# Performance work log

Hardware: AMD Instinct MI355X
Metric: run time of the kernel (lower is better)

Reference implementation:

```python
import jax, jax.numpy as jnp
import numpy as np

B, C, H, W = 8, 512, 32, 32
NH = 8
DH = C // NH
HW = H * W
LN_EPS = 1e-5
NORM_EPS = 1e-12  # torch F.normalize eps


def setup_inputs() -> dict:
    key = jax.random.key(0)
    ks = jax.random.split(key, 8)
    s = 0.02
    return {
        "x": jax.random.normal(ks[0], (B, C, H, W), dtype=jnp.float32),
        "qkv_w": jax.random.normal(ks[1], (3 * C, C), dtype=jnp.float32) * s,
        "proj_w": jax.random.normal(ks[2], (C, C), dtype=jnp.float32) * s,
        "proj_b": jnp.zeros((C,), dtype=jnp.float32),
        "temperature": jnp.ones((NH, 1, 1), dtype=jnp.float32),
        "ln_g": jnp.ones((C,), dtype=jnp.float32),
        "ln_b": jnp.zeros((C,), dtype=jnp.float32),
        "pos_embed": jax.random.normal(ks[3], (1, HW, C), dtype=jnp.float32) * s,
        "dw_w": jax.random.normal(ks[4], (C, 1, 3, 3), dtype=jnp.float32) * s,
        "dw_b": jnp.zeros((C,), dtype=jnp.float32),
        "pw_w": jax.random.normal(ks[5], (C, C, 1, 1), dtype=jnp.float32) * s,
        "pw_b": jnp.zeros((C,), dtype=jnp.float32),
    }


def _l2norm_tokens(t):
    # normalize along token axis (dim=-2), like F.normalize(t, dim=-2)
    n = jnp.sqrt(jnp.sum(t * t, axis=-2, keepdims=True))
    return t / jnp.maximum(n, NORM_EPS)


def _layernorm(t, g, b):
    mu = jnp.mean(t, axis=-1, keepdims=True)
    var = jnp.mean((t - mu) ** 2, axis=-1, keepdims=True)
    return (t - mu) * jax.lax.rsqrt(var + LN_EPS) * g + b


def _dsconv(t, dw_w, dw_b, pw_w, pw_b):
    # depthwise 3x3 SAME + pointwise 1x1, NCHW / OIHW
    y = jax.lax.conv_general_dilated(
        t, dw_w, window_strides=(1, 1), padding="SAME",
        dimension_numbers=("NCHW", "OIHW", "NCHW"), feature_group_count=C)
    y = y + dw_b[None, :, None, None]
    y = jax.lax.conv_general_dilated(
        y, pw_w, window_strides=(1, 1), padding="SAME",
        dimension_numbers=("NCHW", "OIHW", "NCHW"))
    return y + pw_b[None, :, None, None]


def reference(x, qkv_w, proj_w, proj_b, temperature, ln_g, ln_b, pos_embed, dw_w, dw_b, pw_w, pw_b):
    save = x
    t = jnp.transpose(x.reshape(B, C, HW), (0, 2, 1))  # [B, HW, C]
    t = t + pos_embed
    # qkv projection (no bias)
    qkv = t @ qkv_w.T  # [B, HW, 3C]
    qkv = qkv.reshape(B, HW, 3, NH, DH).transpose(2, 0, 3, 1, 4)  # [3,B,NH,HW,DH]
    q, k, v = qkv[0], qkv[1], qkv[2]
    q = _l2norm_tokens(q)
    k = _l2norm_tokens(k)
    attn = jnp.einsum("bhnd,bhmd->bhnm", q, k) * temperature[None]  # [B,NH,HW,HW]
    attn = jax.nn.softmax(attn, axis=-1)
    o = jnp.einsum("bhnm,bhmd->bhnd", attn, v)  # [B,NH,HW,DH]
    o = o.transpose(0, 2, 1, 3).reshape(B, HW, C)
    o = o @ proj_w.T + proj_b
    o = _layernorm(o, ln_g, ln_b)
    o = jnp.transpose(o, (0, 2, 1)).reshape(B, C, H, W)
    o = o + save
    return o + _dsconv(o, dw_w, dw_b, pw_w, pw_b)
```

## Files before the change

kernel.cpp:

```cpp
#include <hip/hip_runtime.h>
#include <math.h>

#define BB_ 8
#define C_ 512
#define C3_ 1536
#define HW_ 1024
#define NH_ 8
#define DH_ 64
#define HH_ 32
#define WW_ 32

typedef __attribute__((ext_vector_type(8))) short short8;
typedef __attribute__((ext_vector_type(4))) short short4v;
typedef __attribute__((ext_vector_type(8))) unsigned short ushort8;
typedef __attribute__((ext_vector_type(4))) unsigned short ushort4_t;
typedef __attribute__((ext_vector_type(4))) float f32x4;
typedef unsigned short ushort;

__device__ inline ushort f2bf(float f) {
  union { float f; unsigned u; } v;
  v.f = f;
  unsigned r = v.u + 0x7fffu + ((v.u >> 16) & 1u);
  return (ushort)(r >> 16);
}
__device__ inline float bf2f(ushort u) {
  union { unsigned u; float f; } v;
  v.u = ((unsigned)u) << 16;
  return v.f;
}

#define GLD16(gptr, lptr)                                                     \
  __builtin_amdgcn_global_load_lds(                                           \
      (const __attribute__((address_space(1))) unsigned int*)(gptr),          \
      (__attribute__((address_space(3))) unsigned int*)(lptr), 16, 0, 0)

__device__ inline f32x4 pv_mfma(const ushort* vp, short4v pf, f32x4 acc) {
#if __has_builtin(__builtin_amdgcn_mfma_f32_16x16x16_bf16)
  short4v vf = *(const short4v*)vp;
  return __builtin_amdgcn_mfma_f32_16x16x16_bf16(vf, pf, acc, 0, 0, 0);
#elif __has_builtin(__builtin_amdgcn_mfma_f32_16x16x16bf16_1k)
  short4v vf = *(const short4v*)vp;
  return __builtin_amdgcn_mfma_f32_16x16x16bf16_1k(vf, pf, acc, 0, 0, 0);
#else
  short4v v4 = *(const short4v*)vp;
  short8 vf = {v4[0], v4[1], v4[2], v4[3], 0, 0, 0, 0};
  short8 pf8 = {pf[0], pf[1], pf[2], pf[3], 0, 0, 0, 0};
  return __builtin_amdgcn_mfma_f32_16x16x32_bf16(vf, pf8, acc, 0, 0, 0);
#endif
}

__global__ __launch_bounds__(256) void prep_kernel(
    const float* __restrict__ x, const float* __restrict__ pos,
    const float* __restrict__ qkv_w, const float* __restrict__ proj_w,
    const float* __restrict__ pw_w, ushort* __restrict__ t,
    ushort* __restrict__ xT, ushort* __restrict__ wts,
    float* __restrict__ sums) {
  const int bid = blockIdx.x;
  const int tid = threadIdx.x;
  if (bid >= 6144) {
    sums[(bid - 6144) * 256 + tid] = 0.f;
    return;
  }
  if (bid >= 1024) {
    int i = (bid - 1024) * 256 + tid;
    if (i < 786432) wts[i] = f2bf(qkv_w[i]);
    else if (i < 1048576) wts[i] = f2bf(proj_w[i - 786432]);
    else wts[i] = f2bf(pw_w[i - 1048576]);
    return;
  }
  __shared__ float tile[64][65];
  const int n0 = (bid & 15) * 64, c0 = ((bid >> 4) & 7) * 64, b = bid >> 7;
#pragma unroll
  for (int it = 0; it < 4; it++) {
    int c_l = (tid >> 4) + it * 16;
    int n_l4 = (tid & 15) * 4;
    float4 v = *(const float4*)&x[((size_t)(b * C_ + c0 + c_l)) * HW_ + n0 + n_l4];
    tile[c_l][n_l4 + 0] = v.x;
    tile[c_l][n_l4 + 1] = v.y;
    tile[c_l][n_l4 + 2] = v.z;
    tile[c_l][n_l4 + 3] = v.w;
  }
  __syncthreads();
#pragma unroll
  for (int it = 0; it < 4; it++) {
    int n_l = (tid >> 4) + it * 16;
    int c_l4 = (tid & 15) * 4;
    size_t token = (size_t)(b * HW_ + n0 + n_l);
    float4 pv = *(const float4*)&pos[(n0 + n_l) * C_ + c0 + c_l4];
    float xv0 = tile[c_l4 + 0][n_l], xv1 = tile[c_l4 + 1][n_l];
    float xv2 = tile[c_l4 + 2][n_l], xv3 = tile[c_l4 + 3][n_l];
    ushort4_t tb = {f2bf(xv0 + pv.x), f2bf(xv1 + pv.y), f2bf(xv2 + pv.z),
                    f2bf(xv3 + pv.w)};
    ushort4_t xb = {f2bf(xv0), f2bf(xv1), f2bf(xv2), f2bf(xv3)};
    *(ushort4_t*)&t[token * C_ + c0 + c_l4] = tb;
    *(ushort4_t*)&xT[token * C_ + c0 + c_l4] = xb;
  }
}

__global__ __launch_bounds__(256) void gemm_qkv(
    const ushort* __restrict__ A, const ushort* __restrict__ Wm,
    ushort* __restrict__ out, ushort* __restrict__ vt,
    float* __restrict__ qsum, float* __restrict__ ksum) {
  const int N = C3_, K = C_;
  __shared__ alignas(16) ushort As[128 * 32];
  __shared__ alignas(16) ushort Bs[128 * 32];
  const int bn = blockIdx.x * 128, bm = blockIdx.y * 128;
  const int tid = threadIdx.x;
  const int w = tid >> 6, lane = tid & 63;
  const int wm = 64 * (w & 1), wn = 64 * (w >> 1);
  const int l15 = lane & 15, lq = lane >> 4;

  f32x4 acc[4][4];
#pragma unroll
  for (int i = 0; i < 4; i++)
#pragma unroll
    for (int j = 0; j < 4; j++) acc[i][j] = (f32x4){0.f, 0.f, 0.f, 0.f};

  const int srr = lane >> 2, sq1 = lane & 3;

  for (int k0 = 0; k0 < K; k0 += 32) {
    __syncthreads();
#pragma unroll
    for (int j = 0; j < 2; j++) {
      int r = 32 * w + 16 * j + srr;
      int q = (sq1 - (r >> 1)) & 3;
      GLD16(A + (size_t)(bm + r) * K + k0 + q * 8, &As[(32 * w + 16 * j) * 32]);
      GLD16(Wm + (size_t)(bn + r) * K + k0 + q * 8, &Bs[(32 * w + 16 * j) * 32]);
    }
    __syncthreads();
    short8 af[4], bf[4];
#pragma unroll
    for (int nt = 0; nt < 4; nt++) {
      int r = wm + nt * 16 + l15;
      af[nt] = *(const short8*)&As[r * 32 + (((lq + (r >> 1)) & 3) * 8)];
      int c = wn + nt * 16 + l15;
      bf[nt] = *(const short8*)&Bs[c * 32 + (((lq + (c >> 1)) & 3) * 8)];
    }
#pragma unroll
    for (int i = 0; i < 4; i++)
#pragma unroll
      for (int j = 0; j < 4; j++)
        acc[i][j] = __builtin_amdgcn_mfma_f32_16x16x32_bf16(af[i], bf[j],
                                                            acc[i][j], 0, 0, 0);
  }

  const int b = bm >> 10;
  if (bn < 1024) {
#pragma unroll
    for (int j = 0; j < 4; j++) {
      int c = bn + wn + j * 16 + l15;
      float ss = 0.f;
#pragma unroll
      for (int i = 0; i < 4; i++) {
#pragma unroll
        for (int r = 0; r < 4; r++) {
          int m = bm + wm + i * 16 + lq * 4 + r;
          float v = acc[i][j][r];
          ss += v * v;
          out[(size_t)m * N + c] = f2bf(v);
        }
      }
      ss += __shfl_xor(ss, 16);
      ss += __shfl_xor(ss, 32);
      if (lq == 0) {
        if (c < 512) atomicAdd(&qsum[b * 512 + c], ss);
        else atomicAdd(&ksum[b * 512 + c - 512], ss);
      }
    }
  } else {
#pragma unroll
    for (int j = 0; j < 4; j++) {
      int c = bn + wn + j * 16 + l15;
      int hd = c - 1024;
      ushort* vrow = vt + ((size_t)(b * 512 + hd)) * HW_;
#pragma unroll
      for (int i = 0; i < 4; i++) {
        int n0 = (bm & 1023) + wm + i * 16 + lq * 4;
        ushort4_t pv = {f2bf(acc[i][j][0]), f2bf(acc[i][j][1]),
                        f2bf(acc[i][j][2]), f2bf(acc[i][j][3])};
        *(ushort4_t*)&vrow[n0] = pv;
      }
    }
  }
}

template <int EPI>
__global__ __launch_bounds__(256) void gemm_n64(
    const ushort* __restrict__ A, const ushort* __restrict__ Wm,
    const float* __restrict__ bias, void* __restrict__ outv,
    const ushort* __restrict__ resid, int N, int K) {
  __shared__ alignas(16) ushort As[128 * 32];
  __shared__ alignas(16) ushort Bs[64 * 32];
  const int bn = blockIdx.x * 64, bm = blockIdx.y * 128;
  const int tid = threadIdx.x;
  const int w = tid >> 6, lane = tid & 63;
  const int wm = 64 * (w & 1), wn = 32 * (w >> 1);
  const int l15 = lane & 15, lq = lane >> 4;

  f32x4 acc[4][2];
#pragma unroll
  for (int i = 0; i < 4; i++)
#pragma unroll
    for (int j = 0; j < 2; j++) acc[i][j] = (f32x4){0.f, 0.f, 0.f, 0.f};

  const int srr = lane >> 2, sq1 = lane & 3;

  for (int k0 = 0; k0 < K; k0 += 32) {
    __syncthreads();
#pragma unroll
    for (int j = 0; j < 2; j++) {
      int r = 32 * w + 16 * j + srr;
      int q = (sq1 - (r >> 1)) & 3;
      GLD16(A + (size_t)(bm + r) * K + k0 + q * 8, &As[(32 * w + 16 * j) * 32]);
    }
    {
      int r = 16 * w + srr;
      int q = (sq1 - (r >> 1)) & 3;
      GLD16(Wm + (size_t)(bn + r) * K + k0 + q * 8, &Bs[(16 * w) * 32]);
    }
    __syncthreads();
    short8 af[4], bf[2];
#pragma unroll
    for (int nt = 0; nt < 4; nt++) {
      int r = wm + nt * 16 + l15;
      af[nt] = *(const short8*)&As[r * 32 + (((lq + (r >> 1)) & 3) * 8)];
    }
#pragma unroll
    for (int j = 0; j < 2; j++) {
      int c = wn + j * 16 + l15;
      bf[j] = *(const short8*)&Bs[c * 32 + (((lq + (c >> 1)) & 3) * 8)];
    }
#pragma unroll
    for (int i = 0; i < 4; i++)
#pragma unroll
      for (int j = 0; j < 2; j++)
        acc[i][j] = __builtin_amdgcn_mfma_f32_16x16x32_bf16(af[i], bf[j],
                                                            acc[i][j], 0, 0, 0);
  }

#pragma unroll
  for (int i = 0; i < 4; i++) {
#pragma unroll
    for (int j = 0; j < 2; j++) {
      int c = bn + wn + j * 16 + l15;
      float bv = bias[c];
#pragma unroll
      for (int r = 0; r < 4; r++) {
        int m = bm + wm + i * 16 + lq * 4 + r;
        float v = acc[i][j][r] + bv;
        if (EPI == 1) {
          ((ushort*)outv)[(size_t)m * N + c] = f2bf(v);
        } else {
          int b = m >> 10, s = m & (HW_ - 1);
          ((float*)outv)[((size_t)(b * C_ + c)) * HW_ + s] =
              v + bf2f(resid[(size_t)m * C_ + c]);
        }
      }
    }
  }
}

__global__ __launch_bounds__(256) void attn_mfma_kernel(
    const ushort* __restrict__ qkv, const ushort* __restrict__ vt,
    const float* __restrict__ qsum, const float* __restrict__ ksum,
    const float* __restrict__ temp, ushort* __restrict__ o) {
  __shared__ alignas(16) ushort Ks[64 * 64];
  __shared__ alignas(16) ushort Vts[64 * 64];
  __shared__ float sc_lds[64];

  const int tid = threadIdx.x;
  const int w = tid >> 6, lane = tid & 63;
  const int quad = lane >> 4, lcol = lane & 15;
  const int bh = blockIdx.x >> 4;
  const int qt = blockIdx.x & 15;
  const int b = bh >> 3, h = bh & 7;
  const int q0 = qt * 64;

  if (tid < 64) {
    float qs = qsum[b * 512 + h * 64 + tid];
    float ks = ksum[b * 512 + h * 64 + tid];
    float iq = 1.0f / fmaxf(sqrtf(qs), 1e-12f);
    float ik = 1.0f / fmaxf(sqrtf(ks), 1e-12f);
    sc_lds[tid] = iq * ik * temp[h];
  }
  __syncthreads();

  short8 qf[2];
  {
    const int m = q0 + w * 16 + lcol;
    const ushort* qrow = qkv + ((size_t)(b * HW_ + m)) * C3_ + h * 64;
#pragma unroll
    for (int kc = 0; kc < 2; kc++) {
      union { short8 v; ushort u[8]; } pk;
#pragma unroll
      for (int j = 0; j < 8; j++) {
        int d = kc * 32 + quad * 8 + j;
        pk.u[j] = f2bf(bf2f(qrow[d]) * sc_lds[d]);
      }
      qf[kc] = pk.v;
    }
  }

  f32x4 ot[4];
#pragma unroll
  for (int dt = 0; dt < 4; dt++) ot[dt] = (f32x4){0.f, 0.f, 0.f, 0.f};
  float lsum = 0.f;

  const ushort* kg = qkv + (size_t)b * HW_ * C3_ + C_ + h * 64;
  const ushort* vg = vt + (size_t)(bh * 64) * HW_;

  const int srow0 = tid >> 3;
  const int sc = tid & 7;

  for (int kt = 0; kt < 16; kt++) {
    __syncthreads();
#pragma unroll
    for (int it = 0; it < 2; it++) {
      int row = srow0 + it * 32;
      int scg = sc ^ (row & 7);
      GLD16(kg + (size_t)(kt * 64 + row) * C3_ + scg * 8,
            &Ks[w * 512 + it * 2048]);
      GLD16(vg + (size_t)row * HW_ + kt * 64 + scg * 8,
            &Vts[w * 512 + it * 2048]);
    }
    __syncthreads();

    f32x4 sfr[4];
#pragma unroll
    for (int nt = 0; nt < 4; nt++) sfr[nt] = (f32x4){0.f, 0.f, 0.f, 0.f};
#pragma unroll
    for (int kc = 0; kc < 2; kc++) {
#pragma unroll
      for (int nt = 0; nt < 4; nt++) {
        int row = nt * 16 + lcol;
        short8 kf = *(const short8*)
            &Ks[row * 64 + (((kc * 4 + quad) ^ (row & 7)) * 8)];
        sfr[nt] =
            __builtin_amdgcn_mfma_f32_16x16x32_bf16(kf, qf[kc], sfr[nt], 0, 0, 0);
      }
    }

    ushort pk[4][4];
#pragma unroll
    for (int nt = 0; nt < 4; nt++) {
#pragma unroll
      for (int r = 0; r < 4; r++) {
        float e = __expf(sfr[nt][r]);
        lsum += e;
        pk[nt][r] = f2bf(e);
      }
    }

#pragma unroll
    for (int nt = 0; nt < 4; nt++) {
      short4v pf = {(short)pk[nt][0], (short)pk[nt][1], (short)pk[nt][2],
                    (short)pk[nt][3]};
      int key = nt * 16 + quad * 4;
#pragma unroll
      for (int dt = 0; dt < 4; dt++) {
        int d = dt * 16 + lcol;
        const ushort* vp =
            &Vts[d * 64 + (((key >> 3) ^ (d & 7)) * 8) + (key & 7)];
        ot[dt] = pv_mfma(vp, pf, ot[dt]);
      }
    }
  }

  lsum += __shfl_xor(lsum, 16);
  lsum += __shfl_xor(lsum, 32);
  const float inv = 1.0f / lsum;

  const int m = q0 + w * 16 + lcol;
  ushort* orow = o + ((size_t)(b * HW_ + m)) * C_ + h * 64;
#pragma unroll
  for (int dt = 0; dt < 4; dt++) {
    ushort4_t pkb = {f2bf(ot[dt][0] * inv), f2bf(ot[dt][1] * inv),
                     f2bf(ot[dt][2] * inv), f2bf(ot[dt][3] * inv)};
    *(ushort4_t*)&orow[dt * 16 + quad * 4] = pkb;
  }
}

__global__ void ln_residual_kernel(const ushort* __restrict__ po,
                                   const ushort* xT,
                                   const float* __restrict__ g,
                                   const float* __restrict__ bb, ushort* ybf) {
  int token = blockIdx.x;
  int t = threadIdx.x;
  const unsigned pv = *(const unsigned*)&po[(size_t)token * C_ + 2 * t];
  float v0 = bf2f((ushort)(pv & 0xffff)), v1 = bf2f((ushort)(pv >> 16));
  float s = v0 + v1;
#pragma unroll
  for (int off = 32; off; off >>= 1) s += __shfl_xor(s, off);
  __shared__ float wr[4];
  if ((t & 63) == 0) wr[t >> 6] = s;
  __syncthreads();
  float mu = (wr[0] + wr[1] + wr[2] + wr[3]) * (1.0f / C_);
  float d0 = v0 - mu, d1 = v1 - mu;
  float vs = d0 * d0 + d1 * d1;
#pragma unroll
  for (int off = 32; off; off >>= 1) vs += __shfl_xor(vs, off);
  __syncthreads();
  if ((t & 63) == 0) wr[t >> 6] = vs;
  __syncthreads();
  float var = (wr[0] + wr[1] + wr[2] + wr[3]) * (1.0f / C_);
  float rstd = rsqrtf(var + 1e-5f);
  const unsigned rv = *(const unsigned*)&xT[(size_t)token * C_ + 2 * t];
  float o0 = d0 * rstd * g[2 * t] + bb[2 * t] + bf2f((ushort)(rv & 0xffff));
  float o1 = d1 * rstd * g[2 * t + 1] + bb[2 * t + 1] + bf2f((ushort)(rv >> 16));
  unsigned ov = (unsigned)f2bf(o0) | ((unsigned)f2bf(o1) << 16);
  *(unsigned*)&ybf[(size_t)token * C_ + 2 * t] = ov;
}

__global__ __launch_bounds__(256) void dwconv_kernel(
    const ushort* __restrict__ y, const float* __restrict__ w,
    const float* __restrict__ bias, ushort* __restrict__ out) {
  const int cg = threadIdx.x & 63, tg = threadIdx.x >> 6;
  const int c0 = cg * 8;
  float wreg[9][8], breg[8];
#pragma unroll
  for (int j = 0; j < 8; j++) {
    breg[j] = bias[c0 + j];
#pragma unroll
    for (int kk = 0; kk < 9; kk++) wreg[kk][j] = w[(c0 + j) * 9 + kk];
  }
  for (int i = 0; i < 4; i++) {
    int token = blockIdx.x * 16 + tg * 4 + i;
    int b = token >> 10, s = token & (HW_ - 1);
    int hh = s >> 5, ww = s & 31;
    float acc[8];
#pragma unroll
    for (int j = 0; j < 8; j++) acc[j] = breg[j];
#pragma unroll
    for (int ky = 0; ky < 3; ky++) {
      int yy = hh + ky - 1;
      if (yy < 0 || yy >= HH_) continue;
#pragma unroll
      for (int kx = 0; kx < 3; kx++) {
        int xx = ww + kx - 1;
        if (xx < 0 || xx >= WW_) continue;
        ushort8 v8 = *(const ushort8*)
            &y[((size_t)(b * HW_ + yy * 32 + xx)) * C_ + c0];
        const float* wk = wreg[ky * 3 + kx];
#pragma unroll
        for (int j = 0; j < 8; j++) acc[j] += wk[j] * bf2f(v8[j]);
      }
    }
    ushort8 pk;
#pragma unroll
    for (int j = 0; j < 8; j++) pk[j] = f2bf(acc[j]);
    *(ushort8*)&out[(size_t)token * C_ + c0] = pk;
  }
}

extern "C" void kernel_launch(void* const* d_in, const int* in_sizes, int n_in,
                              void* d_out, int out_size, void* d_ws,
                              size_t ws_size, hipStream_t stream) {
  const float* x = (const float*)d_in[0];
  const float* qkv_w = (const float*)d_in[1];
  const float* proj_w = (const float*)d_in[2];
  const float* proj_b = (const float*)d_in[3];
  const float* temperature = (const float*)d_in[4];
  const float* ln_g = (const float*)d_in[5];
  const float* ln_b = (const float*)d_in[6];
  const float* pos = (const float*)d_in[7];
  const float* dw_w = (const float*)d_in[8];
  const float* dw_b = (const float*)d_in[9];
  const float* pw_w = (const float*)d_in[10];
  const float* pw_b = (const float*)d_in[11];
  float* out = (float*)d_out;

  float* ws = (float*)d_ws;
  ushort* qkv_bf = (ushort*)ws;
  ushort* t_bf = (ushort*)(ws + (size_t)6 * 1024 * 1024);
  ushort* proj_bf = (ushort*)(ws + (size_t)8 * 1024 * 1024);
  ushort* xT_bf = (ushort*)(ws + (size_t)12 * 1024 * 1024);
  ushort* wts = (ushort*)(ws + (size_t)14 * 1024 * 1024);
  ushort* qkvw_bf = wts;
  ushort* projw_bf = wts + 786432;
  ushort* pww_bf = wts + 1048576;
  float* sums = ws + (size_t)15 * 1024 * 1024;
  float* qsum = sums;
  float* ksum = sums + 4096;
  ushort* vtb = (ushort*)(ws + (size_t)16 * 1024 * 1024);

  const int M = BB_ * HW_;

  prep_kernel<<<6176, 256, 0, stream>>>(x, pos, qkv_w, proj_w, pw_w, t_bf,
                                        xT_bf, wts, sums);
  gemm_qkv<<<dim3(C3_ / 128, M / 128), 256, 0, stream>>>(
      t_bf, qkvw_bf, qkv_bf, vtb, qsum, ksum);
  attn_mfma_kernel<<<BB_ * NH_ * (HW_ / 64), 256, 0, stream>>>(
      qkv_bf, vtb, qsum, ksum, temperature, t_bf);
  gemm_n64<1><<<dim3(C_ / 64, M / 128), 256, 0, stream>>>(
      t_bf, projw_bf, proj_b, proj_bf, nullptr, C_, C_);
  ln_residual_kernel<<<M, 256, 0, stream>>>(proj_bf, xT_bf, ln_g, ln_b,
                                            xT_bf);
  dwconv_kernel<<<M / 16, 256, 0, stream>>>(xT_bf, dw_w, dw_b, t_bf);
  gemm_n64<2><<<dim3(C_ / 64, M / 128), 256, 0, stream>>>(
      t_bf, pww_bf, pw_b, out, xT_bf, C_, C_);
}
```

Baseline: 213.8 us.

## Double-buffer K/V tiles in attention and use one wave per token in LayerNorm

```diff
diff --git a/kernel.cpp b/kernel.cpp
--- a/kernel.cpp
+++ b/kernel.cpp
@@ -264,8 +264,8 @@
     const ushort* __restrict__ qkv, const ushort* __restrict__ vt,
     const float* __restrict__ qsum, const float* __restrict__ ksum,
     const float* __restrict__ temp, ushort* __restrict__ o) {
-  __shared__ alignas(16) ushort Ks[64 * 64];
-  __shared__ alignas(16) ushort Vts[64 * 64];
+  __shared__ alignas(16) ushort Ks[2][64 * 64];
+  __shared__ alignas(16) ushort Vts[2][64 * 64];
   __shared__ float sc_lds[64];
 
   const int tid = threadIdx.x;
@@ -283,6 +283,20 @@
     float ik = 1.0f / fmaxf(sqrtf(ks), 1e-12f);
     sc_lds[tid] = iq * ik * temp[h];
   }
+
+  const ushort* kg = qkv + (size_t)b * HW_ * C3_ + C_ + h * 64;
+  const ushort* vg = vt + (size_t)(bh * 64) * HW_;
+
+  const int srow0 = tid >> 3;
+  const int sc = tid & 7;
+
+#pragma unroll
+  for (int it = 0; it < 2; it++) {
+    int row = srow0 + it * 32;
+    int scg = sc ^ (row & 7);
+    GLD16(kg + (size_t)row * C3_ + scg * 8, &Ks[0][w * 512 + it * 2048]);
+    GLD16(vg + (size_t)row * HW_ + scg * 8, &Vts[0][w * 512 + it * 2048]);
+  }
   __syncthreads();
 
   short8 qf[2];
@@ -306,24 +320,21 @@
   for (int dt = 0; dt < 4; dt++) ot[dt] = (f32x4){0.f, 0.f, 0.f, 0.f};
   float lsum = 0.f;
 
-  const ushort* kg = qkv + (size_t)b * HW_ * C3_ + C_ + h * 64;
-  const ushort* vg = vt + (size_t)(bh * 64) * HW_;
-
-  const int srow0 = tid >> 3;
-  const int sc = tid & 7;
-
   for (int kt = 0; kt < 16; kt++) {
-    __syncthreads();
-#pragma unroll
-    for (int it = 0; it < 2; it++) {
-      int row = srow0 + it * 32;
-      int scg = sc ^ (row & 7);
-      GLD16(kg + (size_t)(kt * 64 + row) * C3_ + scg * 8,
-            &Ks[w * 512 + it * 2048]);
-      GLD16(vg + (size_t)row * HW_ + kt * 64 + scg * 8,
-            &Vts[w * 512 + it * 2048]);
-    }
-    __syncthreads();
+    if (kt > 0) __syncthreads();
+    const int cur = kt & 1;
+    if (kt + 1 < 16) {
+      const int nxt = cur ^ 1;
+#pragma unroll
+      for (int it = 0; it < 2; it++) {
+        int row = srow0 + it * 32;
+        int scg = sc ^ (row & 7);
+        GLD16(kg + (size_t)((kt + 1) * 64 + row) * C3_ + scg * 8,
+              &Ks[nxt][w * 512 + it * 2048]);
+        GLD16(vg + (size_t)row * HW_ + (kt + 1) * 64 + scg * 8,
+              &Vts[nxt][w * 512 + it * 2048]);
+      }
+    }
 
     f32x4 sfr[4];
 #pragma unroll
@@ -334,7 +345,7 @@
       for (int nt = 0; nt < 4; nt++) {
         int row = nt * 16 + lcol;
         short8 kf = *(const short8*)
-            &Ks[row * 64 + (((kc * 4 + quad) ^ (row & 7)) * 8)];
+            &Ks[cur][row * 64 + (((kc * 4 + quad) ^ (row & 7)) * 8)];
         sfr[nt] =
             __builtin_amdgcn_mfma_f32_16x16x32_bf16(kf, qf[kc], sfr[nt], 0, 0, 0);
       }
@@ -360,7 +371,7 @@
       for (int dt = 0; dt < 4; dt++) {
         int d = dt * 16 + lcol;
         const ushort* vp =
-            &Vts[d * 64 + (((key >> 3) ^ (d & 7)) * 8) + (key & 7)];
+            &Vts[cur][d * 64 + (((key >> 3) ^ (d & 7)) * 8) + (key & 7)];
         ot[dt] = pv_mfma(vp, pf, ot[dt]);
       }
     }
@@ -380,35 +391,42 @@
   }
 }
 
-__global__ void ln_residual_kernel(const ushort* __restrict__ po,
-                                   const ushort* xT,
-                                   const float* __restrict__ g,
-                                   const float* __restrict__ bb, ushort* ybf) {
-  int token = blockIdx.x;
-  int t = threadIdx.x;
-  const unsigned pv = *(const unsigned*)&po[(size_t)token * C_ + 2 * t];
-  float v0 = bf2f((ushort)(pv & 0xffff)), v1 = bf2f((ushort)(pv >> 16));
-  float s = v0 + v1;
+__global__ __launch_bounds__(256) void ln_residual_kernel(
+    const ushort* __restrict__ po, const ushort* xT,
+    const float* __restrict__ g, const float* __restrict__ bb, ushort* ybf) {
+  const int wv = threadIdx.x >> 6, lane = threadIdx.x & 63;
+  const int token = blockIdx.x * 4 + wv;
+  const int c0 = lane * 8;
+  ushort8 p8 = *(const ushort8*)&po[(size_t)token * C_ + c0];
+  float v[8];
+  float s = 0.f;
+#pragma unroll
+  for (int j = 0; j < 8; j++) {
+    v[j] = bf2f(p8[j]);
+    s += v[j];
+  }
 #pragma unroll
   for (int off = 32; off; off >>= 1) s += __shfl_xor(s, off);
-  __shared__ float wr[4];
-  if ((t & 63) == 0) wr[t >> 6] = s;
-  __syncthreads();
-  float mu = (wr[0] + wr[1] + wr[2] + wr[3]) * (1.0f / C_);
-  float d0 = v0 - mu, d1 = v1 - mu;
-  float vs = d0 * d0 + d1 * d1;
+  float mu = s * (1.0f / C_);
+  float vs = 0.f;
+#pragma unroll
+  for (int j = 0; j < 8; j++) {
+    v[j] -= mu;
+    vs += v[j] * v[j];
+  }
 #pragma unroll
   for (int off = 32; off; off >>= 1) vs += __shfl_xor(vs, off);
-  __syncthreads();
-  if ((t & 63) == 0) wr[t >> 6] = vs;
-  __syncthreads();
-  float var = (wr[0] + wr[1] + wr[2] + wr[3]) * (1.0f / C_);
-  float rstd = rsqrtf(var + 1e-5f);
-  const unsigned rv = *(const unsigned*)&xT[(size_t)token * C_ + 2 * t];
-  float o0 = d0 * rstd * g[2 * t] + bb[2 * t] + bf2f((ushort)(rv & 0xffff));
-  float o1 = d1 * rstd * g[2 * t + 1] + bb[2 * t + 1] + bf2f((ushort)(rv >> 16));
-  unsigned ov = (unsigned)f2bf(o0) | ((unsigned)f2bf(o1) << 16);
-  *(unsigned*)&ybf[(size_t)token * C_ + 2 * t] = ov;
+  float rstd = rsqrtf(vs * (1.0f / C_) + 1e-5f);
+  float4 g0 = *(const float4*)&g[c0], g1 = *(const float4*)&g[c0 + 4];
+  float4 b0 = *(const float4*)&bb[c0], b1 = *(const float4*)&bb[c0 + 4];
+  ushort8 r8 = *(const ushort8*)&xT[(size_t)token * C_ + c0];
+  float gg[8] = {g0.x, g0.y, g0.z, g0.w, g1.x, g1.y, g1.z, g1.w};
+  float bbv[8] = {b0.x, b0.y, b0.z, b0.w, b1.x, b1.y, b1.z, b1.w};
+  ushort8 pk;
+#pragma unroll
+  for (int j = 0; j < 8; j++)
+    pk[j] = f2bf(v[j] * rstd * gg[j] + bbv[j] + bf2f(r8[j]));
+  *(ushort8*)&ybf[(size_t)token * C_ + c0] = pk;
 }
 
 __global__ __launch_bounds__(256) void dwconv_kernel(
@@ -493,8 +511,8 @@
       qkv_bf, vtb, qsum, ksum, temperature, t_bf);
   gemm_n64<1><<<dim3(C_ / 64, M / 128), 256, 0, stream>>>(
       t_bf, projw_bf, proj_b, proj_bf, nullptr, C_, C_);
-  ln_residual_kernel<<<M, 256, 0, stream>>>(proj_bf, xT_bf, ln_g, ln_b,
-                                            xT_bf);
+  ln_residual_kernel<<<M / 4, 256, 0, stream>>>(proj_bf, xT_bf, ln_g, ln_b,
+                                                xT_bf);
   dwconv_kernel<<<M / 16, 256, 0, stream>>>(xT_bf, dw_w, dw_b, t_bf);
   gemm_n64<2><<<dim3(C_ / 64, M / 128), 256, 0, stream>>>(
       t_bf, pww_bf, pw_b, out, xT_bf, C_, C_);
```

Measured after the change: 210.6 us. No clear change (-1.5%).
